# Kernel optimization log

Measured on AMD Instinct MI355X. Metric: run time of the kernel, lower is better.

## Reference

```python
import math
import jax, jax.numpy as jnp
import numpy as np

DIM = 512
HEADS = 8
B, N = 4, 2048


def _linear_params(key, d_in, d_out):
    # torch nn.Linear default init: U(-1/sqrt(d_in), 1/sqrt(d_in))
    k1, k2 = jax.random.split(key)
    bound = 1.0 / math.sqrt(d_in)
    W = jax.random.uniform(k1, (d_out, d_in), minval=-bound, maxval=bound, dtype=jnp.float32)
    b = jax.random.uniform(k2, (d_out,), minval=-bound, maxval=bound, dtype=jnp.float32)
    return W, b


def setup_inputs() -> dict:
    key = jax.random.key(0)
    kq, kv, km, k1, k2, k3, k4 = jax.random.split(key, 7)
    Q = jax.random.normal(kq, (B, N, DIM), dtype=jnp.float32)
    V = jax.random.normal(kv, (B, N, DIM), dtype=jnp.float32)
    mask = jax.random.bernoulli(km, 0.9, (B, N))  # bool [B, Nk]
    Wq, bq = _linear_params(k1, DIM, DIM)
    Wk, bk = _linear_params(k2, DIM, DIM)
    Wv, bv = _linear_params(k3, DIM, DIM)
    Wo, bo = _linear_params(k4, DIM, DIM)
    return {"Q": Q, "V": V, "mask": mask,
            "Wq": Wq, "bq": bq, "Wk": Wk, "bk": bk,
            "Wv": Wv, "bv": bv, "Wo": Wo, "bo": bo}


def reference(Q, V, mask, Wq, bq, Wk, bk, Wv, bv, Wo, bo):
    Bb, Nq, _ = Q.shape
    dv = Wq.shape[0]
    h = HEADS
    d = dv // h
    q = Q @ Wq.T + bq          # [B, Nq, dv]
    k = V @ Wk.T + bk          # [B, Nk, dv]
    v = V @ Wv.T + bv          # [B, Nk, dv]
    # split heads: torch.cat(split(dim_split, dim=2), dim=0) == head-major stacking
    qh = q.reshape(Bb, Nq, h, d).transpose(2, 0, 1, 3)   # [h, B, Nq, d]
    kh = k.reshape(Bb, -1, h, d).transpose(2, 0, 1, 3)   # [h, B, Nk, d]
    vh = v.reshape(Bb, -1, h, d).transpose(2, 0, 1, 3)   # [h, B, Nk, d]
    # NOTE: original scales by sqrt(Q.shape[-1]) AFTER projection == sqrt(dim_V)
    logits = jnp.einsum('hbqd,hbkd->hbqk', qh, kh) / math.sqrt(dv)
    logits = jnp.where(mask[None, :, None, :], logits, jnp.float32(-100.0))
    A = jax.nn.softmax(logits, axis=-1)
    Oh = qh + jnp.einsum('hbqk,hbkd->hbqd', A, vh)       # residual inside attention
    O = Oh.transpose(1, 2, 0, 3).reshape(Bb, Nq, dv)     # merge heads
    return O + jax.nn.relu(O @ Wo.T + bo)
```

## Files before the change

### kernel.cpp

```cpp
#include <hip/hip_runtime.h>


typedef __attribute__((ext_vector_type(8))) __bf16 bf16x8;
typedef __attribute__((ext_vector_type(4))) float f32x4;

#define DEV static __device__ __forceinline__

constexpr int DIMC = 512;
constexpr int NTOK = 2048;
constexpr int BB   = 4;
constexpr int MTOK = BB * NTOK;
constexpr float SCALE2 = 0.04419417382415922f * 1.4426950408889634f;

DEV unsigned short f2b(float f) {
  unsigned u = __float_as_uint(f);
  u = (u + 0x7FFFu + ((u >> 16) & 1u)) >> 16;
  return (unsigned short)u;
}
DEV float b2f(unsigned short b) { return __uint_as_float(((unsigned)b) << 16); }

DEV unsigned cvtpk(float a, float b) {
  unsigned r;
  asm("v_cvt_pk_bf16_f32 %0, %1, %2" : "=v"(r) : "v"(a), "v"(b));
  return r;
}

DEV bf16x8 pack8(unsigned d0, unsigned d1, unsigned d2, unsigned d3) {
  union { unsigned u[4]; bf16x8 v; } t;
  t.u[0] = d0; t.u[1] = d1; t.u[2] = d2; t.u[3] = d3;
  return t.v;
}

DEV void async_cp16(const void* src, void* dst) {
  __builtin_amdgcn_global_load_lds(
      (const __attribute__((address_space(1))) void*)(src),
      (__attribute__((address_space(3))) void*)(dst), 16, 0, 0);
}

__global__ void cvt_all(const float* __restrict__ Wq, const float* __restrict__ Wk,
                        const float* __restrict__ Wv, const float* __restrict__ Wo,
                        unsigned short* __restrict__ Wqb, unsigned short* __restrict__ Wkb,
                        unsigned short* __restrict__ Wvb, unsigned short* __restrict__ Wob,
                        const unsigned char* __restrict__ mask, int* __restrict__ flag) {
  if (blockIdx.x == 4096) {
    int any = 0;
    for (int i = threadIdx.x; i < BB * NTOK; i += blockDim.x)
      if ((i & 3) == 1 && mask[i]) any = 1;
    if (any) atomicOr(flag, 1);
    return;
  }
  int i = blockIdx.x * blockDim.x + threadIdx.x;
  int wsel = i >> 16, off = i & 65535;
  const float* s = (wsel == 0) ? Wq : (wsel == 1) ? Wk : (wsel == 2) ? Wv : Wo;
  unsigned short* d = (wsel == 0) ? Wqb : (wsel == 1) ? Wkb : (wsel == 2) ? Wvb : Wob;
  float4 v = reinterpret_cast<const float4*>(s)[off];
  ushort4 o;
  o.x = f2b(v.x); o.y = f2b(v.y); o.z = f2b(v.z); o.w = f2b(v.w);
  reinterpret_cast<ushort4*>(d)[off] = o;
}

__global__ __launch_bounds__(256) void proj_gemm(
    const float* __restrict__ Qf, const float* __restrict__ Vf,
    const unsigned short* __restrict__ Wqb, const unsigned short* __restrict__ Wkb,
    const unsigned short* __restrict__ Wvb,
    const float* __restrict__ bq, const float* __restrict__ bk,
    const float* __restrict__ bv,
    unsigned short* __restrict__ qbf, unsigned short* __restrict__ kbf,
    unsigned short* __restrict__ vtb) {
  __shared__ union {
    struct { float A[2][4096]; unsigned short B[2][4096]; } s;
    unsigned short LT[128 * 136];
  } lds;

  const int region = blockIdx.z;
  const float* Af = (region == 0) ? Qf : Vf;
  const unsigned short* W = (region == 0) ? Wqb : (region == 1) ? Wkb : Wvb;
  const float* bias = (region == 0) ? bq : (region == 1) ? bk : bv;

  const int tid = threadIdx.x;
  const int lane = tid & 63;
  const int w = tid >> 6;
  const int r = lane & 15, g = lane >> 4;
  const int rowB = blockIdx.x * 128;
  const int colB = blockIdx.y * 128;
  const int rw = (w >> 1) * 64, cw = (w & 1) * 64;

  auto stageA = [&](float* dst, int kk) {
#pragma unroll
    for (int i = 0; i < 4; ++i) {
      int off = i * 4096 + tid * 16;
      int row = off >> 7;
      int c = ((off >> 4) & 7) ^ (row & 7);
      async_cp16(Af + (size_t)(rowB + row) * DIMC + kk + c * 4, (char*)dst + off);
    }
  };
  auto stageB = [&](unsigned short* dst, int kk) {
#pragma unroll
    for (int i = 0; i < 2; ++i) {
      int off = i * 4096 + tid * 16;
      int row = off >> 6;
      int c = ((off >> 4) & 3) ^ (row & 3);
      async_cp16(W + (size_t)(colB + row) * DIMC + kk + c * 8, (char*)dst + off);
    }
  };

  f32x4 acc[4][4];
#pragma unroll
  for (int i = 0; i < 4; ++i)
#pragma unroll
    for (int j = 0; j < 4; ++j) acc[i][j] = f32x4{0.f, 0.f, 0.f, 0.f};

  stageA(lds.s.A[0], 0);
  stageB(lds.s.B[0], 0);
  __syncthreads();

  int cur = 0;
  for (int kk = 0; kk < DIMC; kk += 32) {
    if (kk + 32 < DIMC) {
      stageA(lds.s.A[cur ^ 1], kk + 32);
      stageB(lds.s.B[cur ^ 1], kk + 32);
    }
    const char* ap = (const char*)lds.s.A[cur];
    const char* bp = (const char*)lds.s.B[cur];
    bf16x8 af[4], bw[4];
#pragma unroll
    for (int i = 0; i < 4; ++i) {
      int row = rw + i * 16 + r;
      f32x4 lo = *reinterpret_cast<const f32x4*>(
          ap + row * 128 + (((2 * g) ^ (row & 7)) << 4));
      f32x4 hi = *reinterpret_cast<const f32x4*>(
          ap + row * 128 + (((2 * g + 1) ^ (row & 7)) << 4));
      af[i] = pack8(cvtpk(lo[0], lo[1]), cvtpk(lo[2], lo[3]),
                    cvtpk(hi[0], hi[1]), cvtpk(hi[2], hi[3]));
    }
#pragma unroll
    for (int j = 0; j < 4; ++j) {
      int row = cw + j * 16 + r;
      bw[j] = *reinterpret_cast<const bf16x8*>(bp + row * 64 + ((g ^ (row & 3)) * 16));
    }
    __builtin_amdgcn_s_setprio(1);
#pragma unroll
    for (int i = 0; i < 4; ++i)
#pragma unroll
      for (int j = 0; j < 4; ++j)
        acc[i][j] = __builtin_amdgcn_mfma_f32_16x16x32_bf16(af[i], bw[j],
                                                            acc[i][j], 0, 0, 0);
    __builtin_amdgcn_s_setprio(0);
    __syncthreads();
    cur ^= 1;
  }

  if (region != 2) {
    const float sc = (region == 1) ? SCALE2 : 1.0f;
    unsigned short* dst = (region == 1) ? kbf : qbf;
#pragma unroll
    for (int i = 0; i < 4; ++i)
#pragma unroll
      for (int j = 0; j < 4; ++j) {
        int n = colB + cw + j * 16 + r;
        float bn = bias[n];
#pragma unroll
        for (int q = 0; q < 4; ++q) {
          int m = rowB + rw + i * 16 + g * 4 + q;
          dst[(size_t)m * DIMC + n] = f2b((acc[i][j][q] + bn) * sc);
        }
      }
  } else {
#pragma unroll
    for (int i = 0; i < 4; ++i)
#pragma unroll
      for (int j = 0; j < 4; ++j) {
        int nl = cw + j * 16 + r;
        float bn = bias[colB + nl];
        int tl = rw + i * 16 + g * 4;
        ushort4 o;
        o.x = f2b(acc[i][j][0] + bn);
        o.y = f2b(acc[i][j][1] + bn);
        o.z = f2b(acc[i][j][2] + bn);
        o.w = f2b(acc[i][j][3] + bn);
        *reinterpret_cast<ushort4*>(&lds.LT[nl * 136 + tl]) = o;
      }
    __syncthreads();
    int bidx = rowB >> 11, t0 = rowB & 2047;
#pragma unroll
    for (int rd = 0; rd < 8; ++rd) {
      int idx = rd * 256 + tid;
      int dv = idx >> 4, ch = idx & 15;
      int gdv = colB + dv, h = gdv >> 6, dd = gdv & 63;
      ushort4 v0 = *reinterpret_cast<const ushort4*>(&lds.LT[dv * 136 + ch * 8]);
      ushort4 v1 = *reinterpret_cast<const ushort4*>(&lds.LT[dv * 136 + ch * 8 + 4]);
      unsigned short* dst = vtb + (size_t)((bidx * 8 + h) * 64 + dd) * NTOK + t0 + ch * 8;
      reinterpret_cast<ushort4*>(dst)[0] = v0;
      reinterpret_cast<ushort4*>(dst)[1] = v1;
    }
  }
}

__global__ __launch_bounds__(256) void out_gemm(
    const float* __restrict__ Of32, const unsigned short* __restrict__ W,
    const float* __restrict__ bias, float* __restrict__ outf) {
  __shared__ struct { float A[2][2048]; unsigned short B[2][4096]; } lds;

  const int tid = threadIdx.x;
  const int lane = tid & 63;
  const int w = tid >> 6;
  const int r = lane & 15, g = lane >> 4;
  const int rowB = blockIdx.x * 64;
  const int colB = blockIdx.y * 128;
  const int rw = (w >> 1) * 32, cw = (w & 1) * 64;

  auto stageA = [&](float* dst, int kk) {
    int off = tid * 16;
#pragma unroll
    for (int i = 0; i < 2; ++i) {
      int o2 = off + i * 4096;
      int row = o2 >> 7;
      int c = ((o2 >> 4) & 7) ^ (row & 7);
      async_cp16(Of32 + (size_t)(rowB + row) * DIMC + kk + c * 4, (char*)dst + o2);
    }
  };
  auto stageB = [&](unsigned short* dst, int kk) {
#pragma unroll
    for (int i = 0; i < 2; ++i) {
      int off = i * 4096 + tid * 16;
      int row = off >> 6;
      int c = ((off >> 4) & 3) ^ (row & 3);
      async_cp16(W + (size_t)(colB + row) * DIMC + kk + c * 8, (char*)dst + off);
    }
  };

  f32x4 acc[2][4];
#pragma unroll
  for (int i = 0; i < 2; ++i)
#pragma unroll
    for (int j = 0; j < 4; ++j) acc[i][j] = f32x4{0.f, 0.f, 0.f, 0.f};

  stageA(lds.A[0], 0);
  stageB(lds.B[0], 0);
  __syncthreads();

  int cur = 0;
  for (int kk = 0; kk < DIMC; kk += 32) {
    if (kk + 32 < DIMC) {
      stageA(lds.A[cur ^ 1], kk + 32);
      stageB(lds.B[cur ^ 1], kk + 32);
    }
    const char* ap = (const char*)lds.A[cur];
    const char* bp = (const char*)lds.B[cur];
    bf16x8 af[2], bw[4];
#pragma unroll
    for (int i = 0; i < 2; ++i) {
      int row = rw + i * 16 + r;
      f32x4 lo = *reinterpret_cast<const f32x4*>(
          ap + row * 128 + (((2 * g) ^ (row & 7)) << 4));
      f32x4 hi = *reinterpret_cast<const f32x4*>(
          ap + row * 128 + (((2 * g + 1) ^ (row & 7)) << 4));
      af[i] = pack8(cvtpk(lo[0], lo[1]), cvtpk(lo[2], lo[3]),
                    cvtpk(hi[0], hi[1]), cvtpk(hi[2], hi[3]));
    }
#pragma unroll
    for (int j = 0; j < 4; ++j) {
      int row = cw + j * 16 + r;
      bw[j] = *reinterpret_cast<const bf16x8*>(bp + row * 64 + ((g ^ (row & 3)) * 16));
    }
    __builtin_amdgcn_s_setprio(1);
#pragma unroll
    for (int i = 0; i < 2; ++i)
#pragma unroll
      for (int j = 0; j < 4; ++j)
        acc[i][j] = __builtin_amdgcn_mfma_f32_16x16x32_bf16(af[i], bw[j],
                                                            acc[i][j], 0, 0, 0);
    __builtin_amdgcn_s_setprio(0);
    __syncthreads();
    cur ^= 1;
  }

#pragma unroll
  for (int i = 0; i < 2; ++i)
#pragma unroll
    for (int j = 0; j < 4; ++j) {
      int n = colB + cw + j * 16 + r;
      float bn = bias[n];
#pragma unroll
      for (int q = 0; q < 4; ++q) {
        int m = rowB + rw + i * 16 + g * 4 + q;
        float val = acc[i][j][q] + bn;
        outf[(size_t)m * DIMC + n] = Of32[(size_t)m * DIMC + n] + fmaxf(val, 0.f);
      }
    }
}

__global__ __launch_bounds__(512, 2) void attn_kernel(
    const unsigned short* __restrict__ qb, const unsigned short* __restrict__ kb,
    const unsigned short* __restrict__ vt, const unsigned char* __restrict__ mask8,
    const int* __restrict__ flagp, float* __restrict__ Of32) {
  __shared__ unsigned short Kt[2][128 * 64];
  __shared__ unsigned short Vt[2][64 * 128];
  __shared__ float MaskAdd[NTOK];

  const int tid = threadIdx.x;
  const int lane = tid & 63;
  const int w = tid >> 6;
  const int r = lane & 15, g = lane >> 4;
  const int bh = blockIdx.x, b = bh >> 3, h = bh & 7;
  const int q0 = blockIdx.y * 256 + w * 32;
  const size_t rowbase = (size_t)b * NTOK;
  const int flag = *flagp;
  const unsigned* mask32 = (const unsigned*)mask8;

  for (int i = tid; i < NTOK; i += 512) {
    unsigned v = flag ? (unsigned)mask8[b * NTOK + i] : mask32[b * NTOK + i];
    MaskAdd[i] = v ? 0.f : -16384.f;
  }

  bf16x8 aq0[2], aq1[2];
#pragma unroll
  for (int ks = 0; ks < 2; ++ks) {
    aq0[ks] = *reinterpret_cast<const bf16x8*>(
        qb + (rowbase + q0 + r) * DIMC + h * 64 + ks * 32 + g * 8);
    aq1[ks] = *reinterpret_cast<const bf16x8*>(
        qb + (rowbase + q0 + 16 + r) * DIMC + h * 64 + ks * 32 + g * 8);
  }

  const unsigned short* kgb = kb + rowbase * DIMC + h * 64;
  const unsigned short* vgb = vt + (size_t)bh * 64 * NTOK;

  auto stageK = [&](int buf, int kt) {
#pragma unroll
    for (int i = 0; i < 2; ++i) {
      int off = i * 8192 + tid * 16;
      int row = off >> 7;
      int s16 = ((off >> 4) & 7) ^ (row & 7);
      int half = row >> 6, rr = row & 63;
      int ff = rr >> 4, gg = (rr >> 2) & 3, j = rr & 3;
      int tok = half * 64 + 8 * gg + 4 * (ff & 1) + 32 * (ff >> 1) + j;
      async_cp16(kgb + (size_t)(kt + tok) * DIMC + (s16 << 3),
                 (char*)&Kt[buf][0] + off);
    }
  };
  auto stageV = [&](int buf, int kt) {
#pragma unroll
    for (int i = 0; i < 2; ++i) {
      int off = i * 8192 + tid * 16;
      int row = off >> 8;
      int s16 = ((off >> 4) & 15) ^ (row & 15);
      async_cp16(vgb + (size_t)row * NTOK + kt + (s16 << 3),
                 (char*)&Vt[buf][0] + off);
    }
  };

  stageK(0, 0);
  stageV(0, 0);
  __syncthreads();

  float lrun0 = 0.f, lrun1 = 0.f;
  f32x4 oacc0[4], oacc1[4];
#pragma unroll
  for (int f = 0; f < 4; ++f) {
    oacc0[f] = f32x4{0.f, 0.f, 0.f, 0.f};
    oacc1[f] = f32x4{0.f, 0.f, 0.f, 0.f};
  }

  const int kswz = (r & 7) << 4;
  const int vswz = r << 4;

  auto softmax_pa = [&](f32x4 (&s)[8], float& lr, bf16x8 (&pa)[4]) {
#pragma unroll
    for (int f = 0; f < 8; ++f)
#pragma unroll
      for (int j = 0; j < 4; ++j) s[f][j] = __builtin_exp2f(s[f][j]);
    float sf[8];
#pragma unroll
    for (int f = 0; f < 8; ++f)
      sf[f] = (s[f][0] + s[f][1]) + (s[f][2] + s[f][3]);
    lr += ((sf[0] + sf[1]) + (sf[2] + sf[3])) +
          ((sf[4] + sf[5]) + (sf[6] + sf[7]));
#pragma unroll
    for (int ks = 0; ks < 4; ++ks) {
      int F0 = 4 * (ks >> 1) + 2 * (ks & 1);
      pa[ks] = pack8(cvtpk(s[F0][0], s[F0][1]), cvtpk(s[F0][2], s[F0][3]),
                     cvtpk(s[F0 + 1][0], s[F0 + 1][1]),
                     cvtpk(s[F0 + 1][2], s[F0 + 1][3]));
    }
  };

  int cur = 0;
  for (int kt = 0; kt < NTOK; kt += 128) {
    if (kt + 128 < NTOK) {
      stageK(cur ^ 1, kt + 128);
      stageV(cur ^ 1, kt + 128);
    }

    f32x4 s0[8], s1[8];
#pragma unroll
    for (int f = 0; f < 8; ++f) {
      int tb = kt + ((f >> 2) << 6) + 8 * g + 4 * (f & 1) + 32 * ((f >> 1) & 1);
      f32x4 mc = *reinterpret_cast<const f32x4*>(&MaskAdd[tb]);
      s0[f] = mc;
      s1[f] = mc;
    }
    const unsigned char* kp = (const unsigned char*)&Kt[cur][0];
    __builtin_amdgcn_s_setprio(1);
#pragma unroll
    for (int ks = 0; ks < 2; ++ks)
#pragma unroll
      for (int f = 0; f < 8; ++f) {
        bf16x8 kf = *reinterpret_cast<const bf16x8*>(
            kp + (f * 16 + r) * 128 + ((ks * 64 + g * 16) ^ kswz));
        s0[f] = __builtin_amdgcn_mfma_f32_16x16x32_bf16(kf, aq0[ks], s0[f], 0, 0, 0);
        s1[f] = __builtin_amdgcn_mfma_f32_16x16x32_bf16(kf, aq1[ks], s1[f], 0, 0, 0);
      }
    __builtin_amdgcn_s_setprio(0);

    bf16x8 pa0[4], pa1[4];
    softmax_pa(s0, lrun0, pa0);
    softmax_pa(s1, lrun1, pa1);

    const unsigned char* vp = (const unsigned char*)&Vt[cur][0];
    __builtin_amdgcn_s_setprio(1);
#pragma unroll
    for (int ks = 0; ks < 4; ++ks)
#pragma unroll
      for (int f = 0; f < 4; ++f) {
        bf16x8 vf = *reinterpret_cast<const bf16x8*>(
            vp + (f * 16 + r) * 256 + ((ks * 64 + g * 16) ^ vswz));
        oacc0[f] = __builtin_amdgcn_mfma_f32_16x16x32_bf16(pa0[ks], vf, oacc0[f], 0, 0, 0);
        oacc1[f] = __builtin_amdgcn_mfma_f32_16x16x32_bf16(pa1[ks], vf, oacc1[f], 0, 0, 0);
      }
    __builtin_amdgcn_s_setprio(0);

    __syncthreads();
    cur ^= 1;
  }

  lrun0 += __shfl_xor(lrun0, 16);
  lrun0 += __shfl_xor(lrun0, 32);
  lrun1 += __shfl_xor(lrun1, 16);
  lrun1 += __shfl_xor(lrun1, 32);

  auto epilogue = [&](float lr, f32x4 (&oa)[4], int qoff) {
#pragma unroll
    for (int j = 0; j < 4; ++j) {
      float linv = 1.0f / __shfl(lr, (lane & 48) | (g * 4 + j));
      int row = q0 + qoff + g * 4 + j;
#pragma unroll
      for (int f = 0; f < 4; ++f) {
        int col = h * 64 + f * 16 + r;
        size_t idx = (rowbase + row) * DIMC + col;
        Of32[idx] = b2f(qb[idx]) + oa[f][j] * linv;
      }
    }
  };
  epilogue(lrun0, oacc0, 0);
  epilogue(lrun1, oacc1, 16);
}

extern "C" void kernel_launch(void* const* d_in, const int* in_sizes, int n_in,
                              void* d_out, int out_size, void* d_ws, size_t ws_size,
                              hipStream_t stream) {
  const float* Q  = (const float*)d_in[0];
  const float* V  = (const float*)d_in[1];
  const unsigned char* mask = (const unsigned char*)d_in[2];
  const float* Wq = (const float*)d_in[3];
  const float* bq = (const float*)d_in[4];
  const float* Wk = (const float*)d_in[5];
  const float* bk = (const float*)d_in[6];
  const float* Wv = (const float*)d_in[7];
  const float* bv = (const float*)d_in[8];
  const float* Wo = (const float*)d_in[9];
  const float* bo = (const float*)d_in[10];

  char* ws = (char*)d_ws;
  size_t off = 0;
  auto alloc = [&](size_t bytes) -> void* {
    void* p = ws + off;
    off += (bytes + 255) & ~(size_t)255;
    return p;
  };
  int* flag = (int*)alloc(4);
  unsigned short* Wqb = (unsigned short*)alloc((size_t)DIMC * DIMC * 2);
  unsigned short* Wkb = (unsigned short*)alloc((size_t)DIMC * DIMC * 2);
  unsigned short* Wvb = (unsigned short*)alloc((size_t)DIMC * DIMC * 2);
  unsigned short* Wob = (unsigned short*)alloc((size_t)DIMC * DIMC * 2);
  unsigned short* qbf = (unsigned short*)alloc((size_t)MTOK * DIMC * 2);
  unsigned short* kbf = (unsigned short*)alloc((size_t)MTOK * DIMC * 2);
  unsigned short* vtb = (unsigned short*)alloc((size_t)MTOK * DIMC * 2);
  float* Of32 = (float*)alloc((size_t)MTOK * DIMC * 4);

  hipMemsetAsync(flag, 0, 4, stream);

  cvt_all<<<4097, 256, 0, stream>>>(Wq, Wk, Wv, Wo, Wqb, Wkb, Wvb, Wob,
                                    mask, flag);

  proj_gemm<<<dim3(64, 4, 3), 256, 0, stream>>>(
      Q, V, Wqb, Wkb, Wvb, bq, bk, bv, qbf, kbf, vtb);

  attn_kernel<<<dim3(BB * 8, NTOK / 256), 512, 0, stream>>>(
      qbf, kbf, vtb, mask, flag, Of32);

  out_gemm<<<dim3(128, 4), 256, 0, stream>>>(
      Of32, Wob, bo, (float*)d_out);
}
```

Before: 119.0 us.

## Split attention keys across two blocks and merge partial results in a combine kernel

The attention grid gains a z dimension of two, so each block processes half of the key sequence and writes an unnormalised fp32 PV partial and a row-sum partial. A new combine kernel adds the two partials, divides by the summed row sums and adds the residual q. Merging is a plain sum because the softmax never subtracts a running max. The intent is to double the number of blocks so the grid fills the GPU better, and launch bounds are raised to allow more resident blocks per CU. The cost is extra global traffic for the partial buffers plus one more kernel launch. The tighter register budget may also cause spills, and the code relies on the two partial buffers sitting next to each other in the workspace.

```diff
diff --git a/kernel.cpp b/kernel.cpp
--- a/kernel.cpp
+++ b/kernel.cpp
@@ -290,13 +290,14 @@
     }
 }
 
-__global__ __launch_bounds__(512, 2) void attn_kernel(
+__global__ __launch_bounds__(512, 4) void attn_kernel(
     const unsigned short* __restrict__ qb, const unsigned short* __restrict__ kb,
     const unsigned short* __restrict__ vt, const unsigned char* __restrict__ mask8,
-    const int* __restrict__ flagp, float* __restrict__ Of32) {
+    const int* __restrict__ flagp, float* __restrict__ PVp,
+    float* __restrict__ lp) {
   __shared__ unsigned short Kt[2][128 * 64];
   __shared__ unsigned short Vt[2][64 * 128];
-  __shared__ float MaskAdd[NTOK];
+  __shared__ float MaskAdd[1024];
 
   const int tid = threadIdx.x;
   const int lane = tid & 63;
@@ -304,12 +305,17 @@
   const int r = lane & 15, g = lane >> 4;
   const int bh = blockIdx.x, b = bh >> 3, h = bh & 7;
   const int q0 = blockIdx.y * 256 + w * 32;
+  const int kbase = blockIdx.z * 1024;
   const size_t rowbase = (size_t)b * NTOK;
   const int flag = *flagp;
   const unsigned* mask32 = (const unsigned*)mask8;
 
-  for (int i = tid; i < NTOK; i += 512) {
-    unsigned v = flag ? (unsigned)mask8[b * NTOK + i] : mask32[b * NTOK + i];
+  PVp += (size_t)blockIdx.z * MTOK * DIMC;
+  lp  += (size_t)blockIdx.z * 32 * NTOK;
+
+  for (int i = tid; i < 1024; i += 512) {
+    unsigned v = flag ? (unsigned)mask8[b * NTOK + kbase + i]
+                      : mask32[b * NTOK + kbase + i];
     MaskAdd[i] = v ? 0.f : -16384.f;
   }
 
@@ -349,8 +355,8 @@
     }
   };
 
-  stageK(0, 0);
-  stageV(0, 0);
+  stageK(0, kbase);
+  stageV(0, kbase);
   __syncthreads();
 
   float lrun0 = 0.f, lrun1 = 0.f;
@@ -385,8 +391,8 @@
   };
 
   int cur = 0;
-  for (int kt = 0; kt < NTOK; kt += 128) {
-    if (kt + 128 < NTOK) {
+  for (int kt = kbase; kt < kbase + 1024; kt += 128) {
+    if (kt + 128 < kbase + 1024) {
       stageK(cur ^ 1, kt + 128);
       stageV(cur ^ 1, kt + 128);
     }
@@ -394,7 +400,8 @@
     f32x4 s0[8], s1[8];
 #pragma unroll
     for (int f = 0; f < 8; ++f) {
-      int tb = kt + ((f >> 2) << 6) + 8 * g + 4 * (f & 1) + 32 * ((f >> 1) & 1);
+      int tb = (kt - kbase) + ((f >> 2) << 6) + 8 * g + 4 * (f & 1) +
+               32 * ((f >> 1) & 1);
       f32x4 mc = *reinterpret_cast<const f32x4*>(&MaskAdd[tb]);
       s0[f] = mc;
       s1[f] = mc;
@@ -437,22 +444,47 @@
   lrun0 += __shfl_xor(lrun0, 32);
   lrun1 += __shfl_xor(lrun1, 16);
   lrun1 += __shfl_xor(lrun1, 32);
-
-  auto epilogue = [&](float lr, f32x4 (&oa)[4], int qoff) {
+  if (g == 0) {
+    lp[(size_t)bh * NTOK + q0 + r] = lrun0;
+    lp[(size_t)bh * NTOK + q0 + 16 + r] = lrun1;
+  }
+
+  auto epiP = [&](f32x4 (&oa)[4], int qoff) {
 #pragma unroll
     for (int j = 0; j < 4; ++j) {
-      float linv = 1.0f / __shfl(lr, (lane & 48) | (g * 4 + j));
       int row = q0 + qoff + g * 4 + j;
 #pragma unroll
       for (int f = 0; f < 4; ++f) {
         int col = h * 64 + f * 16 + r;
-        size_t idx = (rowbase + row) * DIMC + col;
-        Of32[idx] = b2f(qb[idx]) + oa[f][j] * linv;
+        PVp[(rowbase + row) * DIMC + col] = oa[f][j];
       }
     }
   };
-  epilogue(lrun0, oacc0, 0);
-  epilogue(lrun1, oacc1, 16);
+  epiP(oacc0, 0);
+  epiP(oacc1, 16);
+}
+
+__global__ void combine_kernel(const float* __restrict__ PVp0,
+                               const float* __restrict__ PVp1,
+                               const float* __restrict__ lp0,
+                               const float* __restrict__ lp1,
+                               const unsigned short* __restrict__ qb,
+                               float* __restrict__ Of32) {
+  int i4 = blockIdx.x * blockDim.x + threadIdx.x;
+  int m = i4 >> 7, c4 = i4 & 127;
+  int b = m >> 11, q = m & 2047, h = c4 >> 4;
+  int bh = b * 8 + h;
+  float l = lp0[(size_t)bh * NTOK + q] + lp1[(size_t)bh * NTOK + q];
+  float inv = 1.0f / l;
+  f32x4 v0 = reinterpret_cast<const f32x4*>(PVp0)[i4];
+  f32x4 v1 = reinterpret_cast<const f32x4*>(PVp1)[i4];
+  ushort4 qv = reinterpret_cast<const ushort4*>(qb)[i4];
+  f32x4 o;
+  o[0] = b2f(qv.x) + (v0[0] + v1[0]) * inv;
+  o[1] = b2f(qv.y) + (v0[1] + v1[1]) * inv;
+  o[2] = b2f(qv.z) + (v0[2] + v1[2]) * inv;
+  o[3] = b2f(qv.w) + (v0[3] + v1[3]) * inv;
+  reinterpret_cast<f32x4*>(Of32)[i4] = o;
 }
 
 extern "C" void kernel_launch(void* const* d_in, const int* in_sizes, int n_in,
@@ -485,6 +517,10 @@
   unsigned short* qbf = (unsigned short*)alloc((size_t)MTOK * DIMC * 2);
   unsigned short* kbf = (unsigned short*)alloc((size_t)MTOK * DIMC * 2);
   unsigned short* vtb = (unsigned short*)alloc((size_t)MTOK * DIMC * 2);
+  float* PVp0 = (float*)alloc((size_t)MTOK * DIMC * 4);
+  float* PVp1 = (float*)alloc((size_t)MTOK * DIMC * 4);
+  float* lp0  = (float*)alloc((size_t)32 * NTOK * 4);
+  float* lp1  = (float*)alloc((size_t)32 * NTOK * 4);
   float* Of32 = (float*)alloc((size_t)MTOK * DIMC * 4);
 
   hipMemsetAsync(flag, 0, 4, stream);
@@ -495,8 +531,10 @@
   proj_gemm<<<dim3(64, 4, 3), 256, 0, stream>>>(
       Q, V, Wqb, Wkb, Wvb, bq, bk, bv, qbf, kbf, vtb);
 
-  attn_kernel<<<dim3(BB * 8, NTOK / 256), 512, 0, stream>>>(
-      qbf, kbf, vtb, mask, flag, Of32);
+  attn_kernel<<<dim3(BB * 8, NTOK / 256, 2), 512, 0, stream>>>(
+      qbf, kbf, vtb, mask, flag, PVp0, lp0);
+
+  combine_kernel<<<4096, 256, 0, stream>>>(PVp0, PVp1, lp0, lp1, qbf, Of32);
 
   out_gemm<<<dim3(128, 4), 256, 0, stream>>>(
       Of32, Wob, bo, (float*)d_out);
```

New measurement: 240.2 us. 102% more time.

## Split attention key range across wave groups and reduce partial outputs in LDS

Applied to the files above, without the earlier changes.

Each attention block now covers 128 queries instead of 256, and its 8 waves form two groups that each process half of every 128-key tile (64 keys). The partial output accumulators and row sums from the second group are added into the first group's through shared memory before the epilogue. The grid doubles to 512 blocks, which gives more parallelism across CUs, and launch bounds are raised to allow 4 blocks per SM. In exchange, every K/V tile loaded from global memory now serves half as many queries, and an extra LDS reduction and barrier are added at the end.

```diff
diff --git a/kernel.cpp b/kernel.cpp
--- a/kernel.cpp
+++ b/kernel.cpp
@@ -290,20 +290,22 @@
     }
 }
 
-__global__ __launch_bounds__(512, 2) void attn_kernel(
+__global__ __launch_bounds__(512, 4) void attn_kernel(
     const unsigned short* __restrict__ qb, const unsigned short* __restrict__ kb,
     const unsigned short* __restrict__ vt, const unsigned char* __restrict__ mask8,
     const int* __restrict__ flagp, float* __restrict__ Of32) {
-  __shared__ unsigned short Kt[2][128 * 64];
-  __shared__ unsigned short Vt[2][64 * 128];
+  __shared__ unsigned short Kt[2][2][64 * 64];
+  __shared__ unsigned short Vt[2][2][64 * 64];
   __shared__ float MaskAdd[NTOK];
 
   const int tid = threadIdx.x;
   const int lane = tid & 63;
   const int w = tid >> 6;
+  const int kg = w >> 2;
+  const int wq = w & 3;
   const int r = lane & 15, g = lane >> 4;
   const int bh = blockIdx.x, b = bh >> 3, h = bh & 7;
-  const int q0 = blockIdx.y * 256 + w * 32;
+  const int q0 = blockIdx.y * 128 + wq * 32;
   const size_t rowbase = (size_t)b * NTOK;
   const int flag = *flagp;
   const unsigned* mask32 = (const unsigned*)mask8;
@@ -325,32 +327,30 @@
   const unsigned short* kgb = kb + rowbase * DIMC + h * 64;
   const unsigned short* vgb = vt + (size_t)bh * 64 * NTOK;
 
-  auto stageK = [&](int buf, int kt) {
-#pragma unroll
-    for (int i = 0; i < 2; ++i) {
-      int off = i * 8192 + tid * 16;
-      int row = off >> 7;
-      int s16 = ((off >> 4) & 7) ^ (row & 7);
-      int half = row >> 6, rr = row & 63;
-      int ff = rr >> 4, gg = (rr >> 2) & 3, j = rr & 3;
-      int tok = half * 64 + 8 * gg + 4 * (ff & 1) + 32 * (ff >> 1) + j;
-      async_cp16(kgb + (size_t)(kt + tok) * DIMC + (s16 << 3),
-                 (char*)&Kt[buf][0] + off);
-    }
-  };
-  auto stageV = [&](int buf, int kt) {
-#pragma unroll
-    for (int i = 0; i < 2; ++i) {
-      int off = i * 8192 + tid * 16;
-      int row = off >> 8;
-      int s16 = ((off >> 4) & 15) ^ (row & 15);
-      async_cp16(vgb + (size_t)row * NTOK + kt + (s16 << 3),
-                 (char*)&Vt[buf][0] + off);
-    }
-  };
-
-  stageK(0, 0);
-  stageV(0, 0);
+  auto stageK = [&](int pb, int tile, int kt) {
+    int off = tid * 16;
+    int row = off >> 7;
+    int s16 = ((off >> 4) & 7) ^ (row & 7);
+    int ff = row >> 4, gg = (row >> 2) & 3, j = row & 3;
+    int tok = 8 * gg + 4 * (ff & 1) + 32 * (ff >> 1) + j;
+    async_cp16(kgb + (size_t)(kt + tok) * DIMC + (s16 << 3),
+               (char*)&Kt[pb][tile][0] + off);
+  };
+  auto stageV = [&](int pb, int tile, int kt) {
+    int off = tid * 16;
+    int row = off >> 7;
+    int s16 = ((off >> 4) & 7) ^ (row & 7);
+    async_cp16(vgb + (size_t)row * NTOK + kt + (s16 << 3),
+               (char*)&Vt[pb][tile][0] + off);
+  };
+  auto stagePair = [&](int pb, int p) {
+    stageK(pb, 0, p * 128);
+    stageK(pb, 1, p * 128 + 64);
+    stageV(pb, 0, p * 128);
+    stageV(pb, 1, p * 128 + 64);
+  };
+
+  stagePair(0, 0);
   __syncthreads();
 
   float lrun0 = 0.f, lrun1 = 0.f;
@@ -361,69 +361,65 @@
     oacc1[f] = f32x4{0.f, 0.f, 0.f, 0.f};
   }
 
-  const int kswz = (r & 7) << 4;
-  const int vswz = r << 4;
-
-  auto softmax_pa = [&](f32x4 (&s)[8], float& lr, bf16x8 (&pa)[4]) {
-#pragma unroll
-    for (int f = 0; f < 8; ++f)
+  const int swz = (r & 7) << 4;
+
+  auto softmax_pa = [&](f32x4 (&s)[4], float& lr, bf16x8 (&pa)[2]) {
+#pragma unroll
+    for (int f = 0; f < 4; ++f)
 #pragma unroll
       for (int j = 0; j < 4; ++j) s[f][j] = __builtin_exp2f(s[f][j]);
-    float sf[8];
-#pragma unroll
-    for (int f = 0; f < 8; ++f)
+    float sf[4];
+#pragma unroll
+    for (int f = 0; f < 4; ++f)
       sf[f] = (s[f][0] + s[f][1]) + (s[f][2] + s[f][3]);
-    lr += ((sf[0] + sf[1]) + (sf[2] + sf[3])) +
-          ((sf[4] + sf[5]) + (sf[6] + sf[7]));
-#pragma unroll
-    for (int ks = 0; ks < 4; ++ks) {
-      int F0 = 4 * (ks >> 1) + 2 * (ks & 1);
-      pa[ks] = pack8(cvtpk(s[F0][0], s[F0][1]), cvtpk(s[F0][2], s[F0][3]),
-                     cvtpk(s[F0 + 1][0], s[F0 + 1][1]),
-                     cvtpk(s[F0 + 1][2], s[F0 + 1][3]));
-    }
+    lr += (sf[0] + sf[1]) + (sf[2] + sf[3]);
+#pragma unroll
+    for (int ks = 0; ks < 2; ++ks)
+      pa[ks] = pack8(cvtpk(s[2 * ks][0], s[2 * ks][1]),
+                     cvtpk(s[2 * ks][2], s[2 * ks][3]),
+                     cvtpk(s[2 * ks + 1][0], s[2 * ks + 1][1]),
+                     cvtpk(s[2 * ks + 1][2], s[2 * ks + 1][3]));
   };
 
   int cur = 0;
-  for (int kt = 0; kt < NTOK; kt += 128) {
-    if (kt + 128 < NTOK) {
-      stageK(cur ^ 1, kt + 128);
-      stageV(cur ^ 1, kt + 128);
-    }
-
-    f32x4 s0[8], s1[8];
-#pragma unroll
-    for (int f = 0; f < 8; ++f) {
-      int tb = kt + ((f >> 2) << 6) + 8 * g + 4 * (f & 1) + 32 * ((f >> 1) & 1);
+  for (int p = 0; p < NTOK / 128; ++p) {
+    if (p + 1 < NTOK / 128) stagePair(cur ^ 1, p + 1);
+
+    const int kt = p * 128 + kg * 64;
+
+    f32x4 s0[4], s1[4];
+#pragma unroll
+    for (int f = 0; f < 4; ++f) {
+      int tb = kt + 8 * g + 4 * (f & 1) + 32 * (f >> 1);
       f32x4 mc = *reinterpret_cast<const f32x4*>(&MaskAdd[tb]);
       s0[f] = mc;
       s1[f] = mc;
     }
-    const unsigned char* kp = (const unsigned char*)&Kt[cur][0];
+    const unsigned char* kp = (const unsigned char*)&Kt[cur][kg][0];
     __builtin_amdgcn_s_setprio(1);
 #pragma unroll
     for (int ks = 0; ks < 2; ++ks)
 #pragma unroll
-      for (int f = 0; f < 8; ++f) {
+      for (int f = 0; f < 4; ++f) {
         bf16x8 kf = *reinterpret_cast<const bf16x8*>(
-            kp + (f * 16 + r) * 128 + ((ks * 64 + g * 16) ^ kswz));
+            kp + (f * 16 + r) * 128 + ((ks * 64 + g * 16) ^ swz));
         s0[f] = __builtin_amdgcn_mfma_f32_16x16x32_bf16(kf, aq0[ks], s0[f], 0, 0, 0);
         s1[f] = __builtin_amdgcn_mfma_f32_16x16x32_bf16(kf, aq1[ks], s1[f], 0, 0, 0);
       }
     __builtin_amdgcn_s_setprio(0);
 
-    bf16x8 pa0[4], pa1[4];
+    bf16x8 pa0[2], pa1[2];
     softmax_pa(s0, lrun0, pa0);
     softmax_pa(s1, lrun1, pa1);
 
-    const unsigned char* vp = (const unsigned char*)&Vt[cur][0];
+    const unsigned char* vp = (const unsigned char*)&Vt[cur][kg][0];
     __builtin_amdgcn_s_setprio(1);
 #pragma unroll
-    for (int ks = 0; ks < 4; ++ks)
+    for (int ks = 0; ks < 2; ++ks)
 #pragma unroll
       for (int f = 0; f < 4; ++f) {
         bf16x8 vf = *reinterpret_cast<const bf16x8*>(
-            vp + (f * 16 + r) * 256 + ((ks * 64 + g * 16) ^ vswz));
+            vp + (f * 16 + r) * 128 + ((ks * 64 + g * 16) ^ swz));
         oacc0[f] = __builtin_amdgcn_mfma_f32_16x16x32_bf16(pa0[ks], vf, oacc0[f], 0, 0, 0);
         oacc1[f] = __builtin_amdgcn_mfma_f32_16x16x32_bf16(pa1[ks], vf, oacc1[f], 0, 0, 0);
       }
@@ -438,21 +434,45 @@
   lrun1 += __shfl_xor(lrun1, 16);
   lrun1 += __shfl_xor(lrun1, 32);
 
-  auto epilogue = [&](float lr, f32x4 (&oa)[4], int qoff) {
-#pragma unroll
-    for (int j = 0; j < 4; ++j) {
-      float linv = 1.0f / __shfl(lr, (lane & 48) | (g * 4 + j));
-      int row = q0 + qoff + g * 4 + j;
-#pragma unroll
-      for (int f = 0; f < 4; ++f) {
-        int col = h * 64 + f * 16 + r;
-        size_t idx = (rowbase + row) * DIMC + col;
-        Of32[idx] = b2f(qb[idx]) + oa[f][j] * linv;
+  f32x4* cb4 = (f32x4*)&Kt[0][0][0];
+  float* cl = (float*)&Vt[0][0][0];
+  if (kg == 1) {
+#pragma unroll
+    for (int f = 0; f < 4; ++f) {
+      cb4[wq * 512 + f * 64 + lane] = oacc0[f];
+      cb4[wq * 512 + (4 + f) * 64 + lane] = oacc1[f];
+    }
+    if (g == 0) {
+      cl[wq * 32 + r] = lrun0;
+      cl[wq * 32 + 16 + r] = lrun1;
+    }
+  }
+  __syncthreads();
+  if (kg == 0) {
+#pragma unroll
+    for (int f = 0; f < 4; ++f) {
+      oacc0[f] += cb4[wq * 512 + f * 64 + lane];
+      oacc1[f] += cb4[wq * 512 + (4 + f) * 64 + lane];
+    }
+    lrun0 += cl[wq * 32 + r];
+    lrun1 += cl[wq * 32 + 16 + r];
+
+    auto epilogue = [&](float lr, f32x4 (&oa)[4], int qoff) {
+#pragma unroll
+      for (int j = 0; j < 4; ++j) {
+        float linv = 1.0f / __shfl(lr, (lane & 48) | (g * 4 + j));
+        int row = q0 + qoff + g * 4 + j;
+#pragma unroll
+        for (int f = 0; f < 4; ++f) {
+          int col = h * 64 + f * 16 + r;
+          size_t idx = (rowbase + row) * DIMC + col;
+          Of32[idx] = b2f(qb[idx]) + oa[f][j] * linv;
+        }
       }
-    }
-  };
-  epilogue(lrun0, oacc0, 0);
-  epilogue(lrun1, oacc1, 16);
+    };
+    epilogue(lrun0, oacc0, 0);
+    epilogue(lrun1, oacc1, 16);
+  }
 }
 
 extern "C" void kernel_launch(void* const* d_in, const int* in_sizes, int n_in,
@@ -495,7 +515,7 @@
   proj_gemm<<<dim3(64, 4, 3), 256, 0, stream>>>(
       Q, V, Wqb, Wkb, Wvb, bq, bk, bv, qbf, kbf, vtb);
 
-  attn_kernel<<<dim3(BB * 8, NTOK / 256), 512, 0, stream>>>(
+  attn_kernel<<<dim3(BB * 8, NTOK / 128), 512, 0, stream>>>(
       qbf, kbf, vtb, mask, flag, Of32);
 
   out_gemm<<<dim3(128, 4), 256, 0, stream>>>(
```

After: 117.6 us. About the same (-1.2%).
